# Performance work log

Hardware: AMD Instinct MI355X
Metric: run time of the kernel (lower is better)

Reference implementation:

```python
import jax, jax.numpy as jnp
import numpy as np

B, L, D, NH, NP = 8, 4096, 384, 8, 4


def setup_inputs() -> dict:
    key = jax.random.key(0)
    ks = jax.random.split(key, 16)
    s = 1.0 / np.sqrt(D)
    f32 = jnp.float32
    inp = {
        'query': jax.random.normal(ks[0], (B, L, D), f32),
        'key':   jax.random.normal(ks[1], (B, L, D), f32),
        'value': jax.random.normal(ks[2], (B, L, D), f32),
        # linear weights stored as [in, out]; x @ W + b
        'Wq': jax.random.normal(ks[3], (D, D), f32) * s,
        'bq': jnp.zeros((D,), f32),
        'Wk': jax.random.normal(ks[4], (D, D), f32) * s,
        'bk': jnp.zeros((D,), f32),
        'Wv': jax.random.normal(ks[5], (D, D), f32) * s,
        'bv': jnp.zeros((D,), f32),
        'Woff': jax.random.normal(ks[6], (D, NH * NP * 2), f32) * s,
        'boff': jnp.zeros((NH * NP * 2,), f32),
        'Wwt': jax.random.normal(ks[7], (D, NH * NP), f32) * s,
        'bwt': jnp.zeros((NH * NP,), f32),
        'Wo': jax.random.normal(ks[8], (D, D), f32) * s,
        'bo': jnp.zeros((D,), f32),
        'num_heads': NH,
        'n_points': NP,
    }
    return inp


def reference(query, key, value, Wq, bq, Wk, bk, Wv, bv, Woff, boff, Wwt, bwt, Wo, bo, num_heads, n_points):
    Bq, Lq, Dm = query.shape
    Lk = key.shape[1]
    Lv = value.shape[1]
    hd = Dm // num_heads
    h = w = int(round(np.sqrt(Lk)))  # original: feature_size = int(sqrt(Lk))

    q = query @ Wq + bq          # computed as in original (only its reshape is used via output path)
    k = key @ Wk + bk            # faithful: k_proj is computed but unused downstream
    v = value @ Wv + bv

    # offsets [B, nH, Lq, nP, 2] and softmax point weights [B, nH, Lq, nP]
    off = (query @ Woff + boff).reshape(Bq, Lq, num_heads, n_points, 2).transpose(0, 2, 1, 3, 4)
    wt = jax.nn.softmax((query @ Wwt + bwt).reshape(Bq, Lq, num_heads, n_points).transpose(0, 2, 1, 3), axis=-1)

    # reference grid: ref[...,0] = x (tiled over rows), ref[...,1] = y (repeated over cols)
    yy = jnp.linspace(0.0, 1.0, h)
    xx = jnp.linspace(0.0, 1.0, w)
    gy, gx = jnp.meshgrid(yy, xx, indexing='ij')
    ref = jnp.stack([gx.reshape(-1), gy.reshape(-1)], axis=-1)  # [L, 2]

    loc = jnp.clip(ref[None, None, :, None, :] + off, 0.0, 1.0)  # [B,nH,Lq,nP,2]
    # NOTE: faithful to source, which multiplies component 0 by (h-1) (its 'h' coord)
    ph = loc[..., 0] * (h - 1)   # row pixel coord, in [0, h-1]
    pw = loc[..., 1] * (w - 1)   # col pixel coord, in [0, w-1]

    y0 = jnp.floor(ph)
    x0 = jnp.floor(pw)
    wy = (ph - y0)[..., None]
    wx = (pw - x0)[..., None]
    y0i = y0.astype(jnp.int32)
    x0i = x0.astype(jnp.int32)
    y1i = jnp.minimum(y0i + 1, h - 1)
    x1i = jnp.minimum(x0i + 1, w - 1)

    vh = v.reshape(Bq, Lv, num_heads, hd).transpose(0, 2, 1, 3)  # [B,nH,Lv,hd]

    def gather(yi, xi):
        idx = (yi * w + xi).reshape(Bq, num_heads, Lq * n_points, 1)
        return jnp.take_along_axis(vh, idx, axis=2).reshape(Bq, num_heads, Lq, n_points, hd)

    # bilinear sample (align_corners=True; coords in-range so zero-padding never triggers)
    sampled = ((1 - wy) * ((1 - wx) * gather(y0i, x0i) + wx * gather(y0i, x1i))
               + wy * ((1 - wx) * gather(y1i, x0i) + wx * gather(y1i, x1i)))

    out = jnp.einsum('bhlp,bhlpd->bhld', wt, sampled)  # weighted point aggregation
    out = out.transpose(0, 2, 1, 3).reshape(Bq, Lq, Dm)
    return out @ Wo + bo  # dropout is identity in eval mode
```

## Files before the change

### kernel.cpp

```cpp
#include <hip/hip_runtime.h>
#include <hip/hip_bf16.h>
#include <stdint.h>

using bf16 = __hip_bfloat16;

typedef __attribute__((ext_vector_type(8))) short short8;
typedef __attribute__((ext_vector_type(4))) float float4v;

namespace {
constexpr int kL  = 4096;
constexpr int kD  = 384;
constexpr int kHD = 48;
constexpr int kGW = 64;
constexpr int kM  = 32768;

constexpr size_t nValue = (size_t)kM * kD;
constexpr size_t nW     = (size_t)kD * kD;
constexpr size_t nWcat  = (size_t)kD * 96;

constexpr size_t oWvt  = 0;
constexpr size_t oWot  = oWvt  + nW * 2;
constexpr size_t oWcat = oWot  + nW * 2;
constexpr size_t oBcat = oWcat + nWcat * 4;
constexpr size_t oVB   = (oBcat + 96 * 4 + 255) & ~size_t(255);
constexpr size_t oProj = oVB   + nValue * 2;
constexpr size_t oAgg  = oProj + (size_t)kM * 96 * 4;
}

__device__ __forceinline__ void load_lds_16(const void* g, void* l) {
  __builtin_amdgcn_global_load_lds((const __attribute__((address_space(1))) void*)g,
                                   (__attribute__((address_space(3))) void*)l,
                                   16, 0, 0);
}

__device__ __forceinline__ short bf16bits(float f) {
  bf16 h = __float2bfloat16(f);
  return *reinterpret_cast<short*>(&h);
}

__device__ __forceinline__ float bf16raw2f(unsigned short u) {
  union { unsigned int i; float f; } c;
  c.i = ((unsigned int)u) << 16;
  return c.f;
}

__global__ void prep_kernel(const float* __restrict__ Wv,
                            const float* __restrict__ Wo,
                            const float* __restrict__ Woff,
                            const float* __restrict__ Wwt,
                            const float* __restrict__ boff,
                            const float* __restrict__ bwt,
                            bf16* __restrict__ Wvt, bf16* __restrict__ Wot,
                            float* __restrict__ Wcat, float* __restrict__ bcat)
{
  size_t i = (size_t)blockIdx.x * 256 + threadIdx.x;
  if (i < nW) {
    const int n = (int)(i / kD), k = (int)(i % kD);
    Wvt[i] = __float2bfloat16(Wv[(size_t)k * kD + n]);
    return;
  }
  i -= nW;
  if (i < nW) {
    const int n = (int)(i / kD), k = (int)(i % kD);
    Wot[i] = __float2bfloat16(Wo[(size_t)k * kD + n]);
    return;
  }
  i -= nW;
  if (i < nWcat) {
    const int k = (int)(i / 96), n = (int)(i % 96);
    Wcat[i] = (n < 64) ? Woff[(size_t)k * 64 + n] : Wwt[(size_t)k * 32 + (n - 64)];
    return;
  }
  i -= nWcat;
  if (i < 96) bcat[i] = (i < 64) ? boff[i] : bwt[i - 64];
}

template<bool A_F32, bool OUT_BF16>
__device__ __forceinline__
void mfma_gemm_body(char* smem, int bid,
                    const void* __restrict__ A, const bf16* __restrict__ Bt,
                    const float* __restrict__ bias, void* __restrict__ Cout)
{
  bf16* sA = (bf16*)smem;
  bf16* sB = (bf16*)(smem + 8192);
  const int tid  = threadIdx.x;
  const int lane = tid & 63;
  const int wave = tid >> 6;
  const int bm = bid / 3, bn = bid % 3;
  const int m0 = bm * 128, n0 = bn * 128;
  const int wm = (wave >> 1) * 64, wn = (wave & 1) * 64;
  const int r16 = lane & 15, quad = lane >> 4;

  float4v acc[4][4];
  #pragma unroll
  for (int i = 0; i < 4; ++i)
    #pragma unroll
    for (int j = 0; j < 4; ++j) acc[i][j] = (float4v){0.f, 0.f, 0.f, 0.f};

  const int c0 = tid, c1 = tid + 256;

  for (int kt = 0; kt < 12; ++kt) {
    const int k0 = kt * 32;
    if (A_F32) {
      const float* Af = (const float*)A;
      #pragma unroll
      for (int r = 0; r < 2; ++r) {
        const int e = tid + r * 256;
        const int row = e >> 2, c = e & 3;
        const float* src = Af + (size_t)(m0 + row) * kD + k0 + c * 8;
        const float4 f0 = *(const float4*)src;
        const float4 f1 = *(const float4*)(src + 4);
        short8 hx;
        hx[0] = bf16bits(f0.x); hx[1] = bf16bits(f0.y);
        hx[2] = bf16bits(f0.z); hx[3] = bf16bits(f0.w);
        hx[4] = bf16bits(f1.x); hx[5] = bf16bits(f1.y);
        hx[6] = bf16bits(f1.z); hx[7] = bf16bits(f1.w);
        *(short8*)((char*)sA + e * 16) = hx;
      }
    } else {
      const bf16* Ab = (const bf16*)A;
      load_lds_16(Ab + (size_t)(m0 + (c0 >> 2)) * kD + k0 + (c0 & 3) * 8, (char*)sA + c0 * 16);
      load_lds_16(Ab + (size_t)(m0 + (c1 >> 2)) * kD + k0 + (c1 & 3) * 8, (char*)sA + c1 * 16);
    }
    load_lds_16(Bt + (size_t)(n0 + (c0 >> 2)) * kD + k0 + (c0 & 3) * 8, (char*)sB + c0 * 16);
    load_lds_16(Bt + (size_t)(n0 + (c1 >> 2)) * kD + k0 + (c1 & 3) * 8, (char*)sB + c1 * 16);
    __syncthreads();

    short8 av[4], bv[4];
    #pragma unroll
    for (int i = 0; i < 4; ++i)
      av[i] = *(const short8*)(sA + (wm + i * 16 + r16) * 32 + quad * 8);
    #pragma unroll
    for (int j = 0; j < 4; ++j)
      bv[j] = *(const short8*)(sB + (wn + j * 16 + r16) * 32 + quad * 8);
    #pragma unroll
    for (int i = 0; i < 4; ++i)
      #pragma unroll
      for (int j = 0; j < 4; ++j)
        acc[i][j] = __builtin_amdgcn_mfma_f32_16x16x32_bf16(av[i], bv[j], acc[i][j], 0, 0, 0);
    __syncthreads();
  }

  #pragma unroll
  for (int j = 0; j < 4; ++j) {
    const int col = n0 + wn + j * 16 + r16;
    const float bj = bias[col];
    #pragma unroll
    for (int i = 0; i < 4; ++i) {
      const int mbase = m0 + wm + i * 16 + quad * 4;
      #pragma unroll
      for (int r = 0; r < 4; ++r) {
        const float val = acc[i][j][r] + bj;
        if (OUT_BF16)
          ((bf16*)Cout)[(size_t)(mbase + r) * kD + col] = __float2bfloat16(val);
        else
          ((float*)Cout)[(size_t)(mbase + r) * kD + col] = val;
      }
    }
  }
}

__device__ __forceinline__
void proj_gemm_body(char* smem, int bid,
                    const float* __restrict__ Q, const float* __restrict__ Wc,
                    const float* __restrict__ bc, float* __restrict__ proj)
{
  float (*sA)[68]  = (float (*)[68])smem;
  float (*sB)[100] = (float (*)[100])(smem + 8704);
  const int tid = threadIdx.x;
  const int m0  = bid * 64;
  const int tm  = tid >> 4, tn = tid & 15;

  float acc[4][6] = {};

  for (int kt = 0; kt < 12; ++kt) {
    const int k0 = kt * 32;
    #pragma unroll
    for (int r = 0; r < 2; ++r) {
      const int e = tid + r * 256;
      const int m = e >> 3, kc = e & 7;
      const float4 f = *(const float4*)(Q + (size_t)(m0 + m) * kD + k0 + kc * 4);
      sA[kc * 4 + 0][m] = f.x;
      sA[kc * 4 + 1][m] = f.y;
      sA[kc * 4 + 2][m] = f.z;
      sA[kc * 4 + 3][m] = f.w;
    }
    #pragma unroll
    for (int r = 0; r < 6; ++r) {
      const int e = tid + r * 256;
      const int k = e / 48, n2 = (e % 48) * 2;
      *(float2*)(&sB[k][n2]) = *(const float2*)(Wc + (size_t)(k0 + k) * 96 + n2);
    }
    __syncthreads();
    #pragma unroll
    for (int k = 0; k < 32; ++k) {
      const float4 a  = *(const float4*)(&sA[k][tm * 4]);
      const float2 b0 = *(const float2*)(&sB[k][tn * 6]);
      const float2 b1 = *(const float2*)(&sB[k][tn * 6 + 2]);
      const float2 b2 = *(const float2*)(&sB[k][tn * 6 + 4]);
      const float av[4] = {a.x, a.y, a.z, a.w};
      const float bb[6] = {b0.x, b0.y, b1.x, b1.y, b2.x, b2.y};
      #pragma unroll
      for (int i = 0; i < 4; ++i)
        #pragma unroll
        for (int j = 0; j < 6; ++j)
          acc[i][j] += av[i] * bb[j];
    }
    __syncthreads();
  }

  #pragma unroll
  for (int j = 0; j < 6; ++j) {
    const int col = tn * 6 + j;
    const float bj = bc[col];
    #pragma unroll
    for (int i = 0; i < 4; ++i)
      proj[(size_t)(m0 + tm * 4 + i) * 96 + col] = acc[i][j] + bj;
  }
}

__global__ __launch_bounds__(256)
void fat_kernel(const float* __restrict__ value, const bf16* __restrict__ Wvt,
                const float* __restrict__ bv,    bf16* __restrict__ vB,
                const float* __restrict__ Q,     const float* __restrict__ Wcat,
                const float* __restrict__ bcat,  float* __restrict__ proj)
{
  __shared__ __align__(16) char smem[21504];
  const int pb = blockIdx.x;
  if (pb < 512) {
    proj_gemm_body(smem, pb, Q, Wcat, bcat, proj);
  } else {
    mfma_gemm_body<true, true>(smem, pb - 512, value, Wvt, bv, vB);
  }
}

__global__ __launch_bounds__(256)
void out_gemm_kernel(const bf16* __restrict__ A, const bf16* __restrict__ Bt,
                     const float* __restrict__ bias, float* __restrict__ Cout)
{
  __shared__ __align__(16) char smem[16384];
  mfma_gemm_body<false, false>(smem, blockIdx.x, A, Bt, bias, Cout);
}

__global__ __launch_bounds__(256)
void sample_kernel(const float* __restrict__ proj, const bf16* __restrict__ v,
                   bf16* __restrict__ agg)
{
  const int b   = blockIdx.x & 7;
  const int idx = blockIdx.x >> 3;
  const int t = threadIdx.x;

  __shared__ float sp[2][96];
  __shared__ int4  soff[2][32];
  __shared__ float4 sbw[2][32];
  __shared__ float swt[2][32];

  if (t < 192) {
    const int tok = t / 96, j = t % 96;
    const int token = b * kL + idx * 2 + tok;
    sp[tok][j] = proj[(size_t)token * 96 + j];
  }
  __syncthreads();

  if (t < 64) {
    const int tok = t >> 5, i = t & 31;
    const int l = idx * 2 + tok;
    const float offx = sp[tok][2 * i];
    const float offy = sp[tok][2 * i + 1];
    const float refx = (float)(l % kGW) * (1.0f / 63.0f);
    const float refy = (float)(l / kGW) * (1.0f / 63.0f);
    const float locx = fminf(fmaxf(refx + offx, 0.f), 1.f);
    const float locy = fminf(fmaxf(refy + offy, 0.f), 1.f);
    const float ph = locx * 63.0f;
    const float pw = locy * 63.0f;
    const float fy = floorf(ph), fx = floorf(pw);
    const int y0 = (int)fy, x0 = (int)fx;
    const int y1 = min(y0 + 1, 63), x1 = min(x0 + 1, 63);
    const float wy = ph - fy, wx = pw - fx;
    soff[tok][i] = make_int4((y0 * kGW + x0) * kD, (y0 * kGW + x1) * kD,
                             (y1 * kGW + x0) * kD, (y1 * kGW + x1) * kD);
    sbw[tok][i] = make_float4((1.f - wy) * (1.f - wx), (1.f - wy) * wx,
                              wy * (1.f - wx),         wy * wx);
  } else if (t < 80) {
    const int u = t - 64, tok = u >> 3, hh = u & 7;
    const float* lg = &sp[tok][64 + hh * 4];
    const float m = fmaxf(fmaxf(lg[0], lg[1]), fmaxf(lg[2], lg[3]));
    float e[4], sum = 0.f;
    #pragma unroll
    for (int p = 0; p < 4; ++p) { e[p] = expf(lg[p] - m); sum += e[p]; }
    const float inv = 1.0f / sum;
    #pragma unroll
    for (int p = 0; p < 4; ++p) swt[tok][hh * 4 + p] = e[p] * inv;
  }
  __syncthreads();

  if (t < 192) {
    const int tok = t / 96, q = t % 96;
    const int h = q / 12, dg = (q % 12) * 4;
    const int l = idx * 2 + tok;
    const int hd = h * kHD + dg;
    const unsigned short* vb = (const unsigned short*)(v + (size_t)b * kL * kD + hd);
    float4v acc = (float4v){0.f, 0.f, 0.f, 0.f};
    #pragma unroll
    for (int p = 0; p < 4; ++p) {
      const int i = h * 4 + p;
      const int4  o  = soff[tok][i];
      const float4 bw = sbw[tok][i];
      const float wt = swt[tok][i];
      const ushort4 u0 = *(const ushort4*)(vb + o.x);
      const ushort4 u1 = *(const ushort4*)(vb + o.y);
      const ushort4 u2 = *(const ushort4*)(vb + o.z);
      const ushort4 u3 = *(const ushort4*)(vb + o.w);
      float4v s;
      s[0] = bw.x * bf16raw2f(u0.x) + bw.y * bf16raw2f(u1.x)
           + bw.z * bf16raw2f(u2.x) + bw.w * bf16raw2f(u3.x);
      s[1] = bw.x * bf16raw2f(u0.y) + bw.y * bf16raw2f(u1.y)
           + bw.z * bf16raw2f(u2.y) + bw.w * bf16raw2f(u3.y);
      s[2] = bw.x * bf16raw2f(u0.z) + bw.y * bf16raw2f(u1.z)
           + bw.z * bf16raw2f(u2.z) + bw.w * bf16raw2f(u3.z);
      s[3] = bw.x * bf16raw2f(u0.w) + bw.y * bf16raw2f(u1.w)
           + bw.z * bf16raw2f(u2.w) + bw.w * bf16raw2f(u3.w);
      #pragma unroll
      for (int d = 0; d < 4; ++d) acc[d] += wt * s[d];
    }
    ushort4 outu;
    outu.x = (unsigned short)bf16bits(acc[0]);
    outu.y = (unsigned short)bf16bits(acc[1]);
    outu.z = (unsigned short)bf16bits(acc[2]);
    outu.w = (unsigned short)bf16bits(acc[3]);
    const int token = b * kL + l;
    *(ushort4*)((unsigned short*)agg + (size_t)token * kD + hd) = outu;
  }
}

extern "C" void kernel_launch(void* const* d_in, const int* in_sizes, int n_in,
                              void* d_out, int out_size, void* d_ws, size_t ws_size,
                              hipStream_t stream)
{
  const float* query = (const float*)d_in[0];
  const float* value = (const float*)d_in[2];
  const float* Wv    = (const float*)d_in[7];
  const float* bv    = (const float*)d_in[8];
  const float* Woff  = (const float*)d_in[9];
  const float* boff  = (const float*)d_in[10];
  const float* Wwt   = (const float*)d_in[11];
  const float* bwt   = (const float*)d_in[12];
  const float* Wo    = (const float*)d_in[13];
  const float* bo    = (const float*)d_in[14];
  float* out = (float*)d_out;

  char* ws = (char*)d_ws;
  bf16*  Wvt  = (bf16*)(ws + oWvt);
  bf16*  Wot  = (bf16*)(ws + oWot);
  float* Wcat = (float*)(ws + oWcat);
  float* bcat = (float*)(ws + oBcat);
  bf16*  vB   = (bf16*)(ws + oVB);
  float* proj = (float*)(ws + oProj);
  bf16*  aggB = (bf16*)(ws + oAgg);

  const size_t prepN = nW + nW + nWcat + 96;
  prep_kernel<<<dim3((unsigned)((prepN + 255) / 256)), 256, 0, stream>>>(
      Wv, Wo, Woff, Wwt, boff, bwt, Wvt, Wot, Wcat, bcat);

  fat_kernel<<<dim3(512 + 768), 256, 0, stream>>>(
      value, Wvt, bv, vB, query, Wcat, bcat, proj);

  sample_kernel<<<dim3(kM / 2), 256, 0, stream>>>(proj, vB, aggB);

  out_gemm_kernel<<<dim3((kM / 128) * 3), 256, 0, stream>>>(aggB, Wot, bo, out);
}
```

Baseline: 296.0 us.

## Compute offset/weight projection with split-bf16 MFMA instead of fp32 FMA

Replaces the scalar fp32 SIMT GEMM for the offset and attention-weight projection with MFMA bf16 instructions. It uses a hi/lo bf16 split of both operands and three MFMAs per tile to keep near-fp32 accuracy. Weights are pre-split and transposed in the prep kernel, and the block tile grows to 128 rows, which halves the proj block count. This cuts ALU time in the fat kernel at the cost of more LDS and three times the MFMA work.

```diff
diff --git a/kernel.cpp b/kernel.cpp
--- a/kernel.cpp
+++ b/kernel.cpp
@@ -16,12 +16,13 @@
 
 constexpr size_t nValue = (size_t)kM * kD;
 constexpr size_t nW     = (size_t)kD * kD;
-constexpr size_t nWcat  = (size_t)kD * 96;
+constexpr size_t nWcat  = (size_t)96 * kD;
 
 constexpr size_t oWvt  = 0;
 constexpr size_t oWot  = oWvt  + nW * 2;
-constexpr size_t oWcat = oWot  + nW * 2;
-constexpr size_t oBcat = oWcat + nWcat * 4;
+constexpr size_t oWch  = oWot  + nW * 2;
+constexpr size_t oWcl  = oWch  + nWcat * 2;
+constexpr size_t oBcat = oWcl  + nWcat * 2;
 constexpr size_t oVB   = (oBcat + 96 * 4 + 255) & ~size_t(255);
 constexpr size_t oProj = oVB   + nValue * 2;
 constexpr size_t oAgg  = oProj + (size_t)kM * 96 * 4;
@@ -51,7 +52,8 @@
                             const float* __restrict__ boff,
                             const float* __restrict__ bwt,
                             bf16* __restrict__ Wvt, bf16* __restrict__ Wot,
-                            float* __restrict__ Wcat, float* __restrict__ bcat)
+                            bf16* __restrict__ Wch, bf16* __restrict__ Wcl,
+                            float* __restrict__ bcat)
 {
   size_t i = (size_t)blockIdx.x * 256 + threadIdx.x;
   if (i < nW) {
@@ -67,8 +69,11 @@
   }
   i -= nW;
   if (i < nWcat) {
-    const int k = (int)(i / 96), n = (int)(i % 96);
-    Wcat[i] = (n < 64) ? Woff[(size_t)k * 64 + n] : Wwt[(size_t)k * 32 + (n - 64)];
+    const int n = (int)(i / kD), k = (int)(i % kD);
+    const float val = (n < 64) ? Woff[(size_t)k * 64 + n] : Wwt[(size_t)k * 32 + (n - 64)];
+    const bf16 h = __float2bfloat16(val);
+    Wch[i] = h;
+    Wcl[i] = __float2bfloat16(val - __bfloat162float(h));
     return;
   }
   i -= nWcat;
@@ -161,76 +166,111 @@
 }
 
 __device__ __forceinline__
-void proj_gemm_body(char* smem, int bid,
-                    const float* __restrict__ Q, const float* __restrict__ Wc,
+void proj_mfma_body(char* smem, int bid,
+                    const float* __restrict__ Q,
+                    const bf16* __restrict__ WhT, const bf16* __restrict__ WlT,
                     const float* __restrict__ bc, float* __restrict__ proj)
 {
-  float (*sA)[68]  = (float (*)[68])smem;
-  float (*sB)[100] = (float (*)[100])(smem + 8704);
-  const int tid = threadIdx.x;
-  const int m0  = bid * 64;
-  const int tm  = tid >> 4, tn = tid & 15;
-
-  float acc[4][6] = {};
+  bf16* sAh = (bf16*)smem;
+  bf16* sAl = (bf16*)(smem + 8192);
+  bf16* sBh = (bf16*)(smem + 16384);
+  bf16* sBl = (bf16*)(smem + 22528);
+  const int tid  = threadIdx.x;
+  const int lane = tid & 63;
+  const int wave = tid >> 6;
+  const int m0 = bid * 128;
+  const int wm = (wave >> 1) * 64, wn = (wave & 1) * 48;
+  const int r16 = lane & 15, quad = lane >> 4;
+
+  float4v acc[4][3];
+  #pragma unroll
+  for (int i = 0; i < 4; ++i)
+    #pragma unroll
+    for (int j = 0; j < 3; ++j) acc[i][j] = (float4v){0.f, 0.f, 0.f, 0.f};
 
   for (int kt = 0; kt < 12; ++kt) {
     const int k0 = kt * 32;
     #pragma unroll
     for (int r = 0; r < 2; ++r) {
       const int e = tid + r * 256;
-      const int m = e >> 3, kc = e & 7;
-      const float4 f = *(const float4*)(Q + (size_t)(m0 + m) * kD + k0 + kc * 4);
-      sA[kc * 4 + 0][m] = f.x;
-      sA[kc * 4 + 1][m] = f.y;
-      sA[kc * 4 + 2][m] = f.z;
-      sA[kc * 4 + 3][m] = f.w;
-    }
-    #pragma unroll
-    for (int r = 0; r < 6; ++r) {
-      const int e = tid + r * 256;
-      const int k = e / 48, n2 = (e % 48) * 2;
-      *(float2*)(&sB[k][n2]) = *(const float2*)(Wc + (size_t)(k0 + k) * 96 + n2);
+      const int row = e >> 2, c = e & 3;
+      const float* src = Q + (size_t)(m0 + row) * kD + k0 + c * 8;
+      const float4 f0 = *(const float4*)src;
+      const float4 f1 = *(const float4*)(src + 4);
+      const float fv[8] = {f0.x, f0.y, f0.z, f0.w, f1.x, f1.y, f1.z, f1.w};
+      short8 hx, lx;
+      #pragma unroll
+      for (int q = 0; q < 8; ++q) {
+        const bf16 h = __float2bfloat16(fv[q]);
+        hx[q] = *reinterpret_cast<const short*>(&h);
+        const bf16 lo = __float2bfloat16(fv[q] - __bfloat162float(h));
+        lx[q] = *reinterpret_cast<const short*>(&lo);
+      }
+      *(short8*)((char*)sAh + e * 16) = hx;
+      *(short8*)((char*)sAl + e * 16) = lx;
+    }
+    {
+      int c = tid;
+      load_lds_16(WhT + (size_t)(c >> 2) * kD + k0 + (c & 3) * 8, (char*)sBh + c * 16);
+      c = tid + 256;
+      if (c < 384) {
+        load_lds_16(WhT + (size_t)(c >> 2) * kD + k0 + (c & 3) * 8, (char*)sBh + c * 16);
+      } else {
+        const int cc = c - 384;
+        load_lds_16(WlT + (size_t)(cc >> 2) * kD + k0 + (cc & 3) * 8, (char*)sBl + cc * 16);
+      }
+      const int cc = tid + 128;
+      load_lds_16(WlT + (size_t)(cc >> 2) * kD + k0 + (cc & 3) * 8, (char*)sBl + cc * 16);
     }
     __syncthreads();
-    #pragma unroll
-    for (int k = 0; k < 32; ++k) {
-      const float4 a  = *(const float4*)(&sA[k][tm * 4]);
-      const float2 b0 = *(const float2*)(&sB[k][tn * 6]);
-      const float2 b1 = *(const float2*)(&sB[k][tn * 6 + 2]);
-      const float2 b2 = *(const float2*)(&sB[k][tn * 6 + 4]);
-      const float av[4] = {a.x, a.y, a.z, a.w};
-      const float bb[6] = {b0.x, b0.y, b1.x, b1.y, b2.x, b2.y};
-      #pragma unroll
-      for (int i = 0; i < 4; ++i)
-        #pragma unroll
-        for (int j = 0; j < 6; ++j)
-          acc[i][j] += av[i] * bb[j];
+
+    short8 avh[4], avl[4];
+    #pragma unroll
+    for (int i = 0; i < 4; ++i) {
+      avh[i] = *(const short8*)(sAh + (wm + i * 16 + r16) * 32 + quad * 8);
+      avl[i] = *(const short8*)(sAl + (wm + i * 16 + r16) * 32 + quad * 8);
+    }
+    #pragma unroll
+    for (int j = 0; j < 3; ++j) {
+      const short8 bvh = *(const short8*)(sBh + (wn + j * 16 + r16) * 32 + quad * 8);
+      const short8 bvl = *(const short8*)(sBl + (wn + j * 16 + r16) * 32 + quad * 8);
+      #pragma unroll
+      for (int i = 0; i < 4; ++i) {
+        acc[i][j] = __builtin_amdgcn_mfma_f32_16x16x32_bf16(avh[i], bvh, acc[i][j], 0, 0, 0);
+        acc[i][j] = __builtin_amdgcn_mfma_f32_16x16x32_bf16(avh[i], bvl, acc[i][j], 0, 0, 0);
+        acc[i][j] = __builtin_amdgcn_mfma_f32_16x16x32_bf16(avl[i], bvh, acc[i][j], 0, 0, 0);
+      }
     }
     __syncthreads();
   }
 
   #pragma unroll
-  for (int j = 0; j < 6; ++j) {
-    const int col = tn * 6 + j;
+  for (int j = 0; j < 3; ++j) {
+    const int col = wn + j * 16 + r16;
     const float bj = bc[col];
     #pragma unroll
-    for (int i = 0; i < 4; ++i)
-      proj[(size_t)(m0 + tm * 4 + i) * 96 + col] = acc[i][j] + bj;
+    for (int i = 0; i < 4; ++i) {
+      const int mbase = m0 + wm + i * 16 + quad * 4;
+      #pragma unroll
+      for (int r = 0; r < 4; ++r)
+        proj[(size_t)(mbase + r) * 96 + col] = acc[i][j][r] + bj;
+    }
   }
 }
 
 __global__ __launch_bounds__(256)
 void fat_kernel(const float* __restrict__ value, const bf16* __restrict__ Wvt,
                 const float* __restrict__ bv,    bf16* __restrict__ vB,
-                const float* __restrict__ Q,     const float* __restrict__ Wcat,
-                const float* __restrict__ bcat,  float* __restrict__ proj)
-{
-  __shared__ __align__(16) char smem[21504];
+                const float* __restrict__ Q,     const bf16* __restrict__ Wch,
+                const bf16* __restrict__ Wcl,    const float* __restrict__ bcat,
+                float* __restrict__ proj)
+{
+  __shared__ __align__(16) char smem[28672];
   const int pb = blockIdx.x;
-  if (pb < 512) {
-    proj_gemm_body(smem, pb, Q, Wcat, bcat, proj);
+  if (pb < 256) {
+    proj_mfma_body(smem, pb, Q, Wch, Wcl, bcat, proj);
   } else {
-    mfma_gemm_body<true, true>(smem, pb - 512, value, Wvt, bv, vB);
+    mfma_gemm_body<true, true>(smem, pb - 256, value, Wvt, bv, vB);
   }
 }
 
@@ -352,7 +392,8 @@
   char* ws = (char*)d_ws;
   bf16*  Wvt  = (bf16*)(ws + oWvt);
   bf16*  Wot  = (bf16*)(ws + oWot);
-  float* Wcat = (float*)(ws + oWcat);
+  bf16*  Wch  = (bf16*)(ws + oWch);
+  bf16*  Wcl  = (bf16*)(ws + oWcl);
   float* bcat = (float*)(ws + oBcat);
   bf16*  vB   = (bf16*)(ws + oVB);
   float* proj = (float*)(ws + oProj);
@@ -360,10 +401,10 @@
 
   const size_t prepN = nW + nW + nWcat + 96;
   prep_kernel<<<dim3((unsigned)((prepN + 255) / 256)), 256, 0, stream>>>(
-      Wv, Wo, Woff, Wwt, boff, bwt, Wvt, Wot, Wcat, bcat);
-
-  fat_kernel<<<dim3(512 + 768), 256, 0, stream>>>(
-      value, Wvt, bv, vB, query, Wcat, bcat, proj);
+      Wv, Wo, Woff, Wwt, boff, bwt, Wvt, Wot, Wch, Wcl, bcat);
+
+  fat_kernel<<<dim3(256 + 768), 256, 0, stream>>>(
+      value, Wvt, bv, vB, query, Wch, Wcl, bcat, proj);
 
   sample_kernel<<<dim3(kM / 2), 256, 0, stream>>>(proj, vB, aggB);
 
```

Measured after the change: 264.5 us. 1.12x faster.
